# Performance work log

Measured on AMD Instinct MI355X. Metric: run time of the kernel, lower is better.

The kernel has to match this reference:

```python
import jax, jax.numpy as jnp
import numpy as np
import math

T = 4096        # block_size / sequence length
E = 2048        # embedding_dim
D = 256         # head_dim


def setup_inputs() -> dict:
    key = jax.random.key(0)
    k_x, k_q, k_k, k_v = jax.random.split(key, 4)
    x = jax.random.normal(k_x, (T, E), dtype=jnp.float32)
    # nn.Linear weights are [out_features, in_features]
    s = 1.0 / math.sqrt(E)
    Wq = jax.random.normal(k_q, (D, E), dtype=jnp.float32) * s
    Wk = jax.random.normal(k_k, (D, E), dtype=jnp.float32) * s
    Wv = jax.random.normal(k_v, (D, E), dtype=jnp.float32) * s
    return {"x": x, "Wq": Wq, "Wk": Wk, "Wv": Wv}


def reference(x, Wq, Wk, Wv):
    # Projections: x @ W.T  (torch Linear, no bias)
    Q = x @ Wq.T            # [T, D]
    K = x @ Wk.T            # [T, D]
    V = x @ Wv.T            # [T, D]
    scale = 1.0 / math.sqrt(Q.shape[-1])
    scores = (Q @ K.T) * scale                      # [T, T]
    causal = jnp.tril(jnp.ones((T, T), dtype=bool))
    scores = jnp.where(causal, scores, jnp.float32(-1e10))
    probs = jax.nn.softmax(scores, axis=-1)         # row softmax (torch legacy dim=1 for 2-D)
    return probs @ V                                # [T, D]
```

## Files before the change

kernel.cpp:

```cpp
#include <hip/hip_runtime.h>
#include <hip/hip_bf16.h>

#define T_DIM 4096
#define E_DIM 2048
#define D_DIM 256

typedef __attribute__((ext_vector_type(4))) float f32x4;
typedef __attribute__((ext_vector_type(8))) short s16x8;

__device__ __forceinline__ unsigned short f2bf(float f) {
  unsigned int u = __float_as_uint(f);
  unsigned int r = (u + 0x7FFFu + ((u >> 16) & 1u)) >> 16;
  return (unsigned short)r;
}
__device__ __forceinline__ float bf2f(unsigned short h) {
  return __uint_as_float(((unsigned int)h) << 16);
}

__device__ __forceinline__ f32x4 mfma16(s16x8 a, s16x8 b, f32x4 c) {
  return __builtin_amdgcn_mfma_f32_16x16x32_bf16(a, b, c, 0, 0, 0);
}

__device__ __forceinline__ void gload_lds16(const void* g, void* l) {
  __builtin_amdgcn_global_load_lds((const __attribute__((address_space(1))) void*)g,
                                   (__attribute__((address_space(3))) void*)l, 16, 0, 0);
}

__device__ __forceinline__ int fbase(int t) {
  int g = t / 3, r = t - 3 * g;
  return 3 * g * (g + 1) / 2 + r * (g + 1);
}

__global__ __launch_bounds__(256) void cvt_kernel(const float* __restrict__ src,
                                                  unsigned short* __restrict__ dst, int n) {
  int i = blockIdx.x * blockDim.x + threadIdx.x;
  if (i * 8 + 8 <= n) {
    float4 a = ((const float4*)src)[i * 2];
    float4 b = ((const float4*)src)[i * 2 + 1];
    uint4 o;
    o.x = (unsigned int)f2bf(a.x) | ((unsigned int)f2bf(a.y) << 16);
    o.y = (unsigned int)f2bf(a.z) | ((unsigned int)f2bf(a.w) << 16);
    o.z = (unsigned int)f2bf(b.x) | ((unsigned int)f2bf(b.y) << 16);
    o.w = (unsigned int)f2bf(b.z) | ((unsigned int)f2bf(b.w) << 16);
    ((uint4*)dst)[i] = o;
  }
}

__global__ __launch_bounds__(256, 3) void qkv_gemm(
    const unsigned short* __restrict__ xb, const unsigned short* __restrict__ wb,
    unsigned short* __restrict__ Qg, unsigned short* __restrict__ Kg,
    unsigned short* __restrict__ Vt) {
  __shared__ __align__(16) unsigned short Al[2][128 * 64];
  __shared__ __align__(16) unsigned short Bl[2][64 * 64];
  int tid = threadIdx.x, wid = tid >> 6, lane = tid & 63;
  int lr = lane & 15, lk = lane >> 4;
  int bi_ = (int)blockIdx.x;
  int xcd = bi_ & 7, kk = bi_ >> 3;
  int mb_ = (kk / 12) * 8 + xcd, nb_ = kk % 12;
  int bm0 = mb_ * 128, bn0 = nb_ * 64;
  int wm = (wid >> 1) * 64, wn = (wid & 1) * 32;

  f32x4 acc[4][2];
#pragma unroll
  for (int m = 0; m < 4; ++m)
#pragma unroll
    for (int n = 0; n < 2; ++n) acc[m][n] = (f32x4){0.f, 0.f, 0.f, 0.f};

#define STAGE_QKV(kt, buf)                                                              \
  {                                                                                     \
    int k0 = (kt)*64;                                                                   \
    _Pragma("unroll") for (int i2 = 0; i2 < 4; ++i2) {                                  \
      int ci = (wid * 4 + i2) * 64 + lane;                                              \
      int row = ci >> 3, cc = ci & 7;                                                   \
      gload_lds16(&xb[(size_t)(bm0 + row) * E_DIM + k0 + ((cc ^ (row & 7)) << 3)],      \
                  &Al[buf][(size_t)(wid * 4 + i2) * 512]);                              \
    }                                                                                   \
    _Pragma("unroll") for (int i2 = 0; i2 < 2; ++i2) {                                  \
      int ci = (wid * 2 + i2) * 64 + lane;                                              \
      int row = ci >> 3, cc = ci & 7;                                                   \
      gload_lds16(&wb[(size_t)(bn0 + row) * E_DIM + k0 + ((cc ^ (row & 7)) << 3)],      \
                  &Bl[buf][(size_t)(wid * 2 + i2) * 512]);                              \
    }                                                                                   \
  }

  STAGE_QKV(0, 0);
  for (int kt = 0; kt < 32; ++kt) {
    int cur = kt & 1;
    __syncthreads();
    if (kt + 1 < 32) STAGE_QKV(kt + 1, cur ^ 1);
    s16x8 af[2][4], bfr[2][2];
#pragma unroll
    for (int c = 0; c < 2; ++c) {
#pragma unroll
      for (int m = 0; m < 4; ++m)
        af[c][m] = *(const s16x8*)&Al[cur][(size_t)(wm + m * 16 + lr) * 64 +
                                           (((c * 4 + lk) ^ (lr & 7)) << 3)];
#pragma unroll
      for (int n = 0; n < 2; ++n)
        bfr[c][n] = *(const s16x8*)&Bl[cur][(size_t)(wn + n * 16 + lr) * 64 +
                                            (((c * 4 + lk) ^ (lr & 7)) << 3)];
    }
#pragma unroll
    for (int c = 0; c < 2; ++c)
#pragma unroll
      for (int m = 0; m < 4; ++m)
#pragma unroll
        for (int n = 0; n < 2; ++n) acc[m][n] = mfma16(af[c][m], bfr[c][n], acc[m][n]);
  }

#pragma unroll
  for (int m = 0; m < 4; ++m) {
    int grow = bm0 + wm + m * 16 + lk * 4;
#pragma unroll
    for (int n = 0; n < 2; ++n) {
      int gcol = bn0 + wn + n * 16 + lr;
      unsigned short h[4];
#pragma unroll
      for (int r = 0; r < 4; ++r) h[r] = f2bf(acc[m][n][r]);
      if (gcol < 256) {
#pragma unroll
        for (int r = 0; r < 4; ++r) Qg[(size_t)(grow + r) * D_DIM + gcol] = h[r];
      } else if (gcol < 512) {
#pragma unroll
        for (int r = 0; r < 4; ++r) Kg[(size_t)(grow + r) * D_DIM + gcol - 256] = h[r];
      } else {
        uint2 w;
        w.x = (unsigned int)h[0] | ((unsigned int)h[1] << 16);
        w.y = (unsigned int)h[2] | ((unsigned int)h[3] << 16);
        *(uint2*)&Vt[(size_t)(gcol - 512) * T_DIM + grow] = w;
      }
    }
  }
#undef STAGE_QKV
}

__global__ __launch_bounds__(256, 2) void attn_kernel(
    const unsigned short* __restrict__ Qg, const unsigned short* __restrict__ Kg,
    const unsigned short* __restrict__ Vt, unsigned short* __restrict__ Opart,
    float* __restrict__ mpart, float* __restrict__ lpart) {
  __shared__ __align__(16) unsigned short Kl[2][32 * 256];
  __shared__ __align__(16) unsigned short Vl[2][256 * 32];
  __shared__ __align__(16) unsigned short Pl[4][16 * 40];

  int b = blockIdx.x;
  int t = (int)sqrtf(6.0f * (float)b + 2.25f);
  if (t > 63) t = 63;
  while (t > 0 && fbase(t) > b) --t;
  while (t < 63 && fbase(t + 1) <= b) ++t;
  int s = b - fbase(t);
  int nt = 2 * t + 2 - 6 * s;
  if (nt > 6) nt = 6;

  int tid = threadIdx.x, wid = tid >> 6, lane = tid & 63;
  int lr = lane & 15, lk = lane >> 4;
  int q0 = t * 64 + wid * 16;
  unsigned short* pl = &Pl[wid][0];

  s16x8 qf[8];
#pragma unroll
  for (int c = 0; c < 8; ++c)
    qf[c] = *(const s16x8*)&Qg[(size_t)(q0 + lr) * D_DIM + c * 32 + lk * 8];

  float m_run = -1e30f, l_run = 0.0f;
  f32x4 Oa[16];
#pragma unroll
  for (int d = 0; d < 16; ++d) Oa[d] = (f32x4){0.f, 0.f, 0.f, 0.f};
  const float scale = 0.0625f;

#define STAGE_KV(j, buf)                                                             \
  {                                                                                  \
    int kv_ = (j)*32;                                                                \
    _Pragma("unroll") for (int i2 = 0; i2 < 4; ++i2) {                               \
      int ci = (wid * 4 + i2) * 64 + lane;                                           \
      int row = ci >> 5, cc = ci & 31;                                               \
      gload_lds16(&Kg[(size_t)(kv_ + row) * D_DIM + ((cc ^ (row & 7)) << 3)],        \
                  &Kl[buf][(size_t)(wid * 4 + i2) * 512]);                           \
    }                                                                                \
    _Pragma("unroll") for (int i2 = 0; i2 < 4; ++i2) {                               \
      int ci = (wid * 4 + i2) * 64 + lane;                                           \
      int rr = ci >> 2, cc = ci & 3;                                                 \
      gload_lds16(&Vt[(size_t)rr * T_DIM + kv_ + ((cc ^ ((rr >> 1) & 3)) << 3)],     \
                  &Vl[buf][(size_t)(wid * 4 + i2) * 512]);                           \
    }                                                                                \
  }

  STAGE_KV(6 * s, 0);
  for (int n = 0; n < nt; ++n) {
    int j = 6 * s + n;
    int kv = j * 32;
    int cur = n & 1;
    __syncthreads();
    if (n + 1 < nt) STAGE_KV(j + 1, cur ^ 1);
    const unsigned short* kl = &Kl[cur][0];
    const unsigned short* vl = &Vl[cur][0];

    f32x4 sa[2];
    sa[0] = (f32x4){0.f, 0.f, 0.f, 0.f};
    sa[1] = (f32x4){0.f, 0.f, 0.f, 0.f};
#pragma unroll
    for (int jb = 0; jb < 2; ++jb) {
      int row = jb * 16 + lr;
#pragma unroll
      for (int c = 0; c < 8; ++c) {
        s16x8 kf = *(const s16x8*)&kl[(size_t)row * 256 + (((c * 4 + lk) ^ (lr & 7)) << 3)];
        sa[jb] = mfma16(kf, qf[c], sa[jb]);
      }
    }

    float tmax = -1e30f;
#pragma unroll
    for (int jb = 0; jb < 2; ++jb) {
#pragma unroll
      for (int r = 0; r < 4; ++r) {
        float v = sa[jb][r] * scale;
        int keyg = kv + jb * 16 + lk * 4 + r;
        if (keyg > q0 + lr) v = -1e30f;
        sa[jb][r] = v;
        tmax = fmaxf(tmax, v);
      }
    }
    tmax = fmaxf(tmax, __shfl_xor(tmax, 16));
    tmax = fmaxf(tmax, __shfl_xor(tmax, 32));
    float m_new = fmaxf(fmaxf(m_run, tmax), -1e29f);
    float alpha = __expf(m_run - m_new);
    float psum = 0.f;
#pragma unroll
    for (int jb = 0; jb < 2; ++jb) {
      float p0 = __expf(sa[jb][0] - m_new);
      float p1 = __expf(sa[jb][1] - m_new);
      float p2 = __expf(sa[jb][2] - m_new);
      float p3 = __expf(sa[jb][3] - m_new);
      psum += (p0 + p1) + (p2 + p3);
      uint2 w;
      w.x = (unsigned int)f2bf(p0) | ((unsigned int)f2bf(p1) << 16);
      w.y = (unsigned int)f2bf(p2) | ((unsigned int)f2bf(p3) << 16);
      *(uint2*)&pl[lr * 40 + jb * 16 + lk * 4] = w;
    }
    psum += __shfl_xor(psum, 16);
    psum += __shfl_xor(psum, 32);
    l_run = l_run * alpha + psum;
    m_run = m_new;
    float al[4];
#pragma unroll
    for (int r = 0; r < 4; ++r) al[r] = __shfl(alpha, lk * 4 + r);
#pragma unroll
    for (int d = 0; d < 16; ++d) {
#pragma unroll
      for (int r = 0; r < 4; ++r) Oa[d][r] *= al[r];
    }

    s16x8 pf = *(const s16x8*)&pl[lr * 40 + lk * 8];
    int vsw = (lk ^ ((lr >> 1) & 3)) << 3;
#pragma unroll
    for (int d = 0; d < 16; ++d) {
      s16x8 vf = *(const s16x8*)&vl[(size_t)(d * 16 + lr) * 32 + vsw];
      Oa[d] = mfma16(pf, vf, Oa[d]);
    }
  }

#pragma unroll
  for (int d = 0; d < 16; ++d) {
    unsigned short h[4];
#pragma unroll
    for (int r = 0; r < 4; ++r) h[r] = f2bf(Oa[d][r]);
    uint2 w;
    w.x = (unsigned int)h[0] | ((unsigned int)h[1] << 16);
    w.y = (unsigned int)h[2] | ((unsigned int)h[3] << 16);
    *(uint2*)&Opart[((size_t)b * 256 + d * 16 + lr) * 64 + wid * 16 + lk * 4] = w;
  }
  if (lane < 16) {
    mpart[(size_t)b * 64 + wid * 16 + lr] = m_run;
    lpart[(size_t)b * 64 + wid * 16 + lr] = l_run;
  }
#undef STAGE_KV
}

__global__ __launch_bounds__(256) void merge_kernel(const unsigned short* __restrict__ Opart,
                                                    const float* __restrict__ mpart,
                                                    const float* __restrict__ lpart,
                                                    float* __restrict__ out) {
  __shared__ float trans[64 * 65];
  int blk = blockIdx.x;
  int t = blk >> 2;
  int d0 = (blk & 3) * 64;
  int q0 = t * 64;
  int ql = threadIdx.x & 63;
  int dg = threadIdx.x >> 6;
  int g = t / 3, r3 = t - 3 * g;
  int base = 3 * g * (g + 1) / 2 + r3 * (g + 1);
  int nb = (t + 3) / 3;

  float M = -1e30f, den = 0.f;
  for (int p = 0; p < nb; ++p) {
    float mp = mpart[(size_t)(base + p) * 64 + ql];
    float lp = lpart[(size_t)(base + p) * 64 + ql];
    float Mn = fmaxf(M, mp);
    float sc = __expf(M - Mn);
    den = den * sc + __expf(mp - Mn) * lp;
    M = Mn;
  }
  float inv = 1.0f / den;

  float acc[16];
#pragma unroll
  for (int k = 0; k < 16; ++k) acc[k] = 0.f;
  for (int p = 0; p < nb; ++p) {
    float w = __expf(mpart[(size_t)(base + p) * 64 + ql] - M);
    const unsigned short* oprow = &Opart[((size_t)(base + p) * 256 + d0 + dg) * 64 + ql];
#pragma unroll
    for (int k = 0; k < 16; ++k) acc[k] += w * bf2f(oprow[(size_t)(4 * k) * 64]);
  }
#pragma unroll
  for (int k = 0; k < 16; ++k) trans[(dg + 4 * k) * 65 + ql] = acc[k] * inv;
  __syncthreads();

#pragma unroll
  for (int k = 0; k < 16; ++k) {
    int qq = (threadIdx.x >> 6) + 4 * k;
    int dd = threadIdx.x & 63;
    out[(size_t)(q0 + qq) * 256 + d0 + dd] = trans[dd * 65 + qq];
  }
}

extern "C" void kernel_launch(void* const* d_in, const int* in_sizes, int n_in,
                              void* d_out, int out_size, void* d_ws, size_t ws_size,
                              hipStream_t stream) {
  const float* x  = (const float*)d_in[0];
  const float* Wq = (const float*)d_in[1];
  const float* Wk = (const float*)d_in[2];
  const float* Wv = (const float*)d_in[3];

  char* ws = (char*)d_ws;
  unsigned short* xb = (unsigned short*)(ws);
  unsigned short* wb = (unsigned short*)(ws + 16777216);
  unsigned short* Qg = (unsigned short*)(ws + 19922944);
  unsigned short* Kg = (unsigned short*)(ws + 22020096);
  unsigned short* Vt = (unsigned short*)(ws + 24117248);
  unsigned short* Opart = (unsigned short*)(ws + 26214400);
  float* mpart = (float*)(ws + 49643520);
  float* lpart = (float*)(ws + 49826560);

  cvt_kernel<<<4096, 256, 0, stream>>>(x, xb, T_DIM * E_DIM);
  cvt_kernel<<<256, 256, 0, stream>>>(Wq, wb, D_DIM * E_DIM);
  cvt_kernel<<<256, 256, 0, stream>>>(Wk, wb + (size_t)D_DIM * E_DIM, D_DIM * E_DIM);
  cvt_kernel<<<256, 256, 0, stream>>>(Wv, wb + (size_t)2 * D_DIM * E_DIM, D_DIM * E_DIM);

  qkv_gemm<<<384, 256, 0, stream>>>(xb, wb, Qg, Kg, Vt);

  attn_kernel<<<715, 256, 0, stream>>>(Qg, Kg, Vt, Opart, mpart, lpart);

  merge_kernel<<<256, 256, 0, stream>>>(Opart, mpart, lpart, (float*)d_out);
}
```

Before: 108.4 us.

## Double attention query tile per warp and fuse conversion kernels into one launch

Each attention wave now handles 32 query rows (two 16-row MFMA blocks) instead of 16, so each K/V fragment loaded from LDS feeds two MFMAs. The block tile grows to 128 queries, the split-KV partition changes to chunks of 5 key tiles (435 blocks), and the merge kernel is adapted to 128-row tiles. A mask-skip check avoids causal masking for tiles fully below the diagonal. The four fp32-to-bf16 conversion launches are merged into a single kernel. The trade-off is doubled accumulator registers and fewer blocks for load balancing.

```diff
diff --git a/kernel.cpp b/kernel.cpp
--- a/kernel.cpp
+++ b/kernel.cpp
@@ -4,6 +4,7 @@
 #define T_DIM 4096
 #define E_DIM 2048
 #define D_DIM 256
+#define NT_SPLIT 5
 
 typedef __attribute__((ext_vector_type(4))) float f32x4;
 typedef __attribute__((ext_vector_type(8))) short s16x8;
@@ -26,24 +27,29 @@
                                    (__attribute__((address_space(3))) void*)l, 16, 0, 0);
 }
 
-__device__ __forceinline__ int fbase(int t) {
-  int g = t / 3, r = t - 3 * g;
-  return 3 * g * (g + 1) / 2 + r * (g + 1);
-}
-
-__global__ __launch_bounds__(256) void cvt_kernel(const float* __restrict__ src,
-                                                  unsigned short* __restrict__ dst, int n) {
-  int i = blockIdx.x * blockDim.x + threadIdx.x;
-  if (i * 8 + 8 <= n) {
-    float4 a = ((const float4*)src)[i * 2];
-    float4 b = ((const float4*)src)[i * 2 + 1];
-    uint4 o;
-    o.x = (unsigned int)f2bf(a.x) | ((unsigned int)f2bf(a.y) << 16);
-    o.y = (unsigned int)f2bf(a.z) | ((unsigned int)f2bf(a.w) << 16);
-    o.z = (unsigned int)f2bf(b.x) | ((unsigned int)f2bf(b.y) << 16);
-    o.w = (unsigned int)f2bf(b.z) | ((unsigned int)f2bf(b.w) << 16);
-    ((uint4*)dst)[i] = o;
-  }
+__global__ __launch_bounds__(256) void cvt_all(const float* __restrict__ x,
+                                               const float* __restrict__ wq,
+                                               const float* __restrict__ wk,
+                                               const float* __restrict__ wv,
+                                               unsigned short* __restrict__ xb,
+                                               unsigned short* __restrict__ wb) {
+  int blk = blockIdx.x;
+  const float* src;
+  unsigned short* dst;
+  int rel;
+  if (blk < 4096)      { src = x;  dst = xb;           rel = blk; }
+  else if (blk < 4352) { src = wq; dst = wb;           rel = blk - 4096; }
+  else if (blk < 4608) { src = wk; dst = wb + 524288;  rel = blk - 4352; }
+  else                 { src = wv; dst = wb + 1048576; rel = blk - 4608; }
+  int i = rel * 256 + threadIdx.x;
+  float4 a = ((const float4*)src)[i * 2];
+  float4 b = ((const float4*)src)[i * 2 + 1];
+  uint4 o;
+  o.x = (unsigned int)f2bf(a.x) | ((unsigned int)f2bf(a.y) << 16);
+  o.y = (unsigned int)f2bf(a.z) | ((unsigned int)f2bf(a.w) << 16);
+  o.z = (unsigned int)f2bf(b.x) | ((unsigned int)f2bf(b.y) << 16);
+  o.w = (unsigned int)f2bf(b.z) | ((unsigned int)f2bf(b.w) << 16);
+  ((uint4*)dst)[i] = o;
 }
 
 __global__ __launch_bounds__(256, 3) void qkv_gemm(
@@ -140,137 +146,167 @@
     float* __restrict__ mpart, float* __restrict__ lpart) {
   __shared__ __align__(16) unsigned short Kl[2][32 * 256];
   __shared__ __align__(16) unsigned short Vl[2][256 * 32];
-  __shared__ __align__(16) unsigned short Pl[4][16 * 40];
+  __shared__ __align__(16) unsigned short Pl[4][32 * 40];
 
   int b = blockIdx.x;
-  int t = (int)sqrtf(6.0f * (float)b + 2.25f);
-  if (t > 63) t = 63;
-  while (t > 0 && fbase(t) > b) --t;
-  while (t < 63 && fbase(t + 1) <= b) ++t;
-  int s = b - fbase(t);
-  int nt = 2 * t + 2 - 6 * s;
-  if (nt > 6) nt = 6;
+  int t = 31, s = 0;
+  {
+    int acc = 0;
+#pragma unroll 1
+    for (int k = 1; k <= 32; ++k) {
+      int c = (4 * k + 4) / 5;
+      if (acc + c > b) { t = k - 1; s = b - acc; break; }
+      acc += c;
+    }
+  }
+  int nt = 4 * (t + 1) - NT_SPLIT * s;
+  if (nt > NT_SPLIT) nt = NT_SPLIT;
 
   int tid = threadIdx.x, wid = tid >> 6, lane = tid & 63;
   int lr = lane & 15, lk = lane >> 4;
-  int q0 = t * 64 + wid * 16;
+  int q0w = t * 128 + wid * 32;
   unsigned short* pl = &Pl[wid][0];
 
-  s16x8 qf[8];
-#pragma unroll
-  for (int c = 0; c < 8; ++c)
-    qf[c] = *(const s16x8*)&Qg[(size_t)(q0 + lr) * D_DIM + c * 32 + lk * 8];
-
-  float m_run = -1e30f, l_run = 0.0f;
-  f32x4 Oa[16];
-#pragma unroll
-  for (int d = 0; d < 16; ++d) Oa[d] = (f32x4){0.f, 0.f, 0.f, 0.f};
+  s16x8 qf[2][8];
+#pragma unroll
+  for (int qb = 0; qb < 2; ++qb)
+#pragma unroll
+    for (int c = 0; c < 8; ++c)
+      qf[qb][c] = *(const s16x8*)&Qg[(size_t)(q0w + qb * 16 + lr) * D_DIM + c * 32 + lk * 8];
+
+  float m_run[2] = {-1e30f, -1e30f}, l_run[2] = {0.f, 0.f};
+  f32x4 Oa[2][16];
+#pragma unroll
+  for (int qb = 0; qb < 2; ++qb)
+#pragma unroll
+    for (int d = 0; d < 16; ++d) Oa[qb][d] = (f32x4){0.f, 0.f, 0.f, 0.f};
   const float scale = 0.0625f;
+  int j0 = NT_SPLIT * s;
 
 #define STAGE_KV(j, buf)                                                             \
   {                                                                                  \
     int kv_ = (j)*32;                                                                \
     _Pragma("unroll") for (int i2 = 0; i2 < 4; ++i2) {                               \
-      int ci = (wid * 4 + i2) * 64 + lane;                                           \
-      int row = ci >> 5, cc = ci & 31;                                               \
-      gload_lds16(&Kg[(size_t)(kv_ + row) * D_DIM + ((cc ^ (row & 7)) << 3)],        \
+      int l = (wid * 4 + i2) * 64 + lane;                                            \
+      int row = l >> 5, gcs = l & 31;                                                \
+      gload_lds16(&Kg[(size_t)(kv_ + row) * D_DIM + ((gcs ^ (row & 7)) << 3)],       \
                   &Kl[buf][(size_t)(wid * 4 + i2) * 512]);                           \
     }                                                                                \
     _Pragma("unroll") for (int i2 = 0; i2 < 4; ++i2) {                               \
-      int ci = (wid * 4 + i2) * 64 + lane;                                           \
-      int rr = ci >> 2, cc = ci & 3;                                                 \
-      gload_lds16(&Vt[(size_t)rr * T_DIM + kv_ + ((cc ^ ((rr >> 1) & 3)) << 3)],     \
+      int l = (wid * 4 + i2) * 64 + lane;                                            \
+      int d_ = l >> 2, gs = l & 3;                                                   \
+      gload_lds16(&Vt[(size_t)d_ * T_DIM + kv_ + ((gs ^ ((d_ >> 1) & 3)) << 3)],     \
                   &Vl[buf][(size_t)(wid * 4 + i2) * 512]);                           \
     }                                                                                \
   }
 
-  STAGE_KV(6 * s, 0);
+  STAGE_KV(j0, 0);
   for (int n = 0; n < nt; ++n) {
-    int j = 6 * s + n;
-    int kv = j * 32;
-    int cur = n & 1;
+    int j = j0 + n, kv = j * 32, cur = n & 1;
     __syncthreads();
     if (n + 1 < nt) STAGE_KV(j + 1, cur ^ 1);
     const unsigned short* kl = &Kl[cur][0];
     const unsigned short* vl = &Vl[cur][0];
 
-    f32x4 sa[2];
-    sa[0] = (f32x4){0.f, 0.f, 0.f, 0.f};
-    sa[1] = (f32x4){0.f, 0.f, 0.f, 0.f};
+    f32x4 sa[2][2];
+#pragma unroll
+    for (int qb = 0; qb < 2; ++qb)
+#pragma unroll
+      for (int jb = 0; jb < 2; ++jb) sa[qb][jb] = (f32x4){0.f, 0.f, 0.f, 0.f};
+    int sw = lr & 7;
 #pragma unroll
     for (int jb = 0; jb < 2; ++jb) {
-      int row = jb * 16 + lr;
+      int rowbase = (jb * 16 + lr) * 32;
 #pragma unroll
       for (int c = 0; c < 8; ++c) {
-        s16x8 kf = *(const s16x8*)&kl[(size_t)row * 256 + (((c * 4 + lk) ^ (lr & 7)) << 3)];
-        sa[jb] = mfma16(kf, qf[c], sa[jb]);
-      }
-    }
-
-    float tmax = -1e30f;
-#pragma unroll
-    for (int jb = 0; jb < 2; ++jb) {
-#pragma unroll
-      for (int r = 0; r < 4; ++r) {
-        float v = sa[jb][r] * scale;
-        int keyg = kv + jb * 16 + lk * 4 + r;
-        if (keyg > q0 + lr) v = -1e30f;
-        sa[jb][r] = v;
-        tmax = fmaxf(tmax, v);
-      }
-    }
-    tmax = fmaxf(tmax, __shfl_xor(tmax, 16));
-    tmax = fmaxf(tmax, __shfl_xor(tmax, 32));
-    float m_new = fmaxf(fmaxf(m_run, tmax), -1e29f);
-    float alpha = __expf(m_run - m_new);
-    float psum = 0.f;
-#pragma unroll
-    for (int jb = 0; jb < 2; ++jb) {
-      float p0 = __expf(sa[jb][0] - m_new);
-      float p1 = __expf(sa[jb][1] - m_new);
-      float p2 = __expf(sa[jb][2] - m_new);
-      float p3 = __expf(sa[jb][3] - m_new);
-      psum += (p0 + p1) + (p2 + p3);
+        s16x8 kf = *(const s16x8*)&kl[(size_t)(rowbase + ((c * 4 + lk) ^ sw)) * 8];
+        sa[0][jb] = mfma16(kf, qf[0][c], sa[0][jb]);
+        sa[1][jb] = mfma16(kf, qf[1][c], sa[1][jb]);
+      }
+    }
+
+    bool needmask = (kv + 31 > q0w);
+    float alpha_s[2];
+#pragma unroll
+    for (int qb = 0; qb < 2; ++qb) {
+      int myq = q0w + qb * 16 + lr;
+      float tmax = -1e30f;
+#pragma unroll
+      for (int jb = 0; jb < 2; ++jb) {
+#pragma unroll
+        for (int r = 0; r < 4; ++r) {
+          float v = sa[qb][jb][r] * scale;
+          if (needmask && (kv + jb * 16 + lk * 4 + r) > myq) v = -1e30f;
+          sa[qb][jb][r] = v;
+          tmax = fmaxf(tmax, v);
+        }
+      }
+      tmax = fmaxf(tmax, __shfl_xor(tmax, 16));
+      tmax = fmaxf(tmax, __shfl_xor(tmax, 32));
+      float m_new = fmaxf(fmaxf(m_run[qb], tmax), -1e29f);
+      alpha_s[qb] = __expf(m_run[qb] - m_new);
+      float psum = 0.f;
+#pragma unroll
+      for (int jb = 0; jb < 2; ++jb) {
+        float p0 = __expf(sa[qb][jb][0] - m_new);
+        float p1 = __expf(sa[qb][jb][1] - m_new);
+        float p2 = __expf(sa[qb][jb][2] - m_new);
+        float p3 = __expf(sa[qb][jb][3] - m_new);
+        psum += (p0 + p1) + (p2 + p3);
+        uint2 w;
+        w.x = (unsigned int)f2bf(p0) | ((unsigned int)f2bf(p1) << 16);
+        w.y = (unsigned int)f2bf(p2) | ((unsigned int)f2bf(p3) << 16);
+        *(uint2*)&pl[(qb * 16 + lr) * 40 + jb * 16 + lk * 4] = w;
+      }
+      psum += __shfl_xor(psum, 16);
+      psum += __shfl_xor(psum, 32);
+      l_run[qb] = l_run[qb] * alpha_s[qb] + psum;
+      m_run[qb] = m_new;
+    }
+
+    float al[2][4];
+#pragma unroll
+    for (int qb = 0; qb < 2; ++qb)
+#pragma unroll
+      for (int r = 0; r < 4; ++r) al[qb][r] = __shfl(alpha_s[qb], lk * 4 + r);
+#pragma unroll
+    for (int qb = 0; qb < 2; ++qb)
+#pragma unroll
+      for (int d = 0; d < 16; ++d) {
+#pragma unroll
+        for (int r = 0; r < 4; ++r) Oa[qb][d][r] *= al[qb][r];
+      }
+
+    s16x8 pf0 = *(const s16x8*)&pl[lr * 40 + lk * 8];
+    s16x8 pf1 = *(const s16x8*)&pl[(16 + lr) * 40 + lk * 8];
+    int vsw = lk ^ ((lr >> 1) & 3);
+#pragma unroll
+    for (int d = 0; d < 16; ++d) {
+      s16x8 vf = *(const s16x8*)&vl[(size_t)((d * 16 + lr) * 4 + vsw) * 8];
+      Oa[0][d] = mfma16(pf0, vf, Oa[0][d]);
+      Oa[1][d] = mfma16(pf1, vf, Oa[1][d]);
+    }
+  }
+
+#pragma unroll
+  for (int d = 0; d < 16; ++d) {
+#pragma unroll
+    for (int qb = 0; qb < 2; ++qb) {
+      unsigned short h[4];
+#pragma unroll
+      for (int r = 0; r < 4; ++r) h[r] = f2bf(Oa[qb][d][r]);
       uint2 w;
-      w.x = (unsigned int)f2bf(p0) | ((unsigned int)f2bf(p1) << 16);
-      w.y = (unsigned int)f2bf(p2) | ((unsigned int)f2bf(p3) << 16);
-      *(uint2*)&pl[lr * 40 + jb * 16 + lk * 4] = w;
-    }
-    psum += __shfl_xor(psum, 16);
-    psum += __shfl_xor(psum, 32);
-    l_run = l_run * alpha + psum;
-    m_run = m_new;
-    float al[4];
-#pragma unroll
-    for (int r = 0; r < 4; ++r) al[r] = __shfl(alpha, lk * 4 + r);
-#pragma unroll
-    for (int d = 0; d < 16; ++d) {
-#pragma unroll
-      for (int r = 0; r < 4; ++r) Oa[d][r] *= al[r];
-    }
-
-    s16x8 pf = *(const s16x8*)&pl[lr * 40 + lk * 8];
-    int vsw = (lk ^ ((lr >> 1) & 3)) << 3;
-#pragma unroll
-    for (int d = 0; d < 16; ++d) {
-      s16x8 vf = *(const s16x8*)&vl[(size_t)(d * 16 + lr) * 32 + vsw];
-      Oa[d] = mfma16(pf, vf, Oa[d]);
-    }
-  }
-
-#pragma unroll
-  for (int d = 0; d < 16; ++d) {
-    unsigned short h[4];
-#pragma unroll
-    for (int r = 0; r < 4; ++r) h[r] = f2bf(Oa[d][r]);
-    uint2 w;
-    w.x = (unsigned int)h[0] | ((unsigned int)h[1] << 16);
-    w.y = (unsigned int)h[2] | ((unsigned int)h[3] << 16);
-    *(uint2*)&Opart[((size_t)b * 256 + d * 16 + lr) * 64 + wid * 16 + lk * 4] = w;
-  }
-  if (lane < 16) {
-    mpart[(size_t)b * 64 + wid * 16 + lr] = m_run;
-    lpart[(size_t)b * 64 + wid * 16 + lr] = l_run;
+      w.x = (unsigned int)h[0] | ((unsigned int)h[1] << 16);
+      w.y = (unsigned int)h[2] | ((unsigned int)h[3] << 16);
+      *(uint2*)&Opart[((size_t)b * 256 + d * 16 + lr) * 128 + wid * 32 + qb * 16 + lk * 4] = w;
+    }
+  }
+  if (lk == 0) {
+#pragma unroll
+    for (int qb = 0; qb < 2; ++qb) {
+      mpart[(size_t)b * 128 + wid * 32 + qb * 16 + lr] = m_run[qb];
+      lpart[(size_t)b * 128 + wid * 32 + qb * 16 + lr] = l_run[qb];
+    }
   }
 #undef STAGE_KV
 }
@@ -279,46 +315,43 @@
                                                     const float* __restrict__ mpart,
                                                     const float* __restrict__ lpart,
                                                     float* __restrict__ out) {
-  __shared__ float trans[64 * 65];
+  __shared__ float trans[128 * 65];
   int blk = blockIdx.x;
-  int t = blk >> 2;
-  int d0 = (blk & 3) * 64;
-  int q0 = t * 64;
-  int ql = threadIdx.x & 63;
-  int dg = threadIdx.x >> 6;
-  int g = t / 3, r3 = t - 3 * g;
-  int base = 3 * g * (g + 1) / 2 + r3 * (g + 1);
-  int nb = (t + 3) / 3;
+  int t = blk >> 2, d0 = (blk & 3) * 64, q0 = t * 128;
+  int ql = threadIdx.x & 127, dg = threadIdx.x >> 7;
+  int base = 0;
+#pragma unroll 1
+  for (int k = 1; k <= t; ++k) base += (4 * k + 4) / 5;
+  int nb = (4 * (t + 1) + 4) / 5;
 
   float M = -1e30f, den = 0.f;
   for (int p = 0; p < nb; ++p) {
-    float mp = mpart[(size_t)(base + p) * 64 + ql];
-    float lp = lpart[(size_t)(base + p) * 64 + ql];
+    float mp = mpart[(size_t)(base + p) * 128 + ql];
+    float lp = lpart[(size_t)(base + p) * 128 + ql];
     float Mn = fmaxf(M, mp);
-    float sc = __expf(M - Mn);
-    den = den * sc + __expf(mp - Mn) * lp;
+    den = den * __expf(M - Mn) + __expf(mp - Mn) * lp;
     M = Mn;
   }
   float inv = 1.0f / den;
 
-  float acc[16];
-#pragma unroll
-  for (int k = 0; k < 16; ++k) acc[k] = 0.f;
+  float acc[32];
+#pragma unroll
+  for (int k = 0; k < 32; ++k) acc[k] = 0.f;
   for (int p = 0; p < nb; ++p) {
-    float w = __expf(mpart[(size_t)(base + p) * 64 + ql] - M);
-    const unsigned short* oprow = &Opart[((size_t)(base + p) * 256 + d0 + dg) * 64 + ql];
-#pragma unroll
-    for (int k = 0; k < 16; ++k) acc[k] += w * bf2f(oprow[(size_t)(4 * k) * 64]);
-  }
-#pragma unroll
-  for (int k = 0; k < 16; ++k) trans[(dg + 4 * k) * 65 + ql] = acc[k] * inv;
+    float w = __expf(mpart[(size_t)(base + p) * 128 + ql] - M);
+    const unsigned short* op = &Opart[((size_t)(base + p) * 256 + d0 + dg) * 128 + ql];
+#pragma unroll
+    for (int k = 0; k < 32; ++k) acc[k] += w * bf2f(op[(size_t)(2 * k) * 128]);
+  }
+#pragma unroll
+  for (int k = 0; k < 32; ++k) trans[ql * 65 + dg + 2 * k] = acc[k] * inv;
   __syncthreads();
 
 #pragma unroll
-  for (int k = 0; k < 16; ++k) {
-    int qq = (threadIdx.x >> 6) + 4 * k;
+  for (int kk = 0; kk < 32; ++kk) {
+    int q = (threadIdx.x >> 6) + 4 * kk;
     int dd = threadIdx.x & 63;
-    out[(size_t)(q0 + qq) * 256 + d0 + dd] = trans[dd * 65 + qq];
+    out[(size_t)(q0 + q) * 256 + d0 + dd] = trans[q * 65 + dd];
   }
 }
 
@@ -337,17 +370,11 @@
   unsigned short* Kg = (unsigned short*)(ws + 22020096);
   unsigned short* Vt = (unsigned short*)(ws + 24117248);
   unsigned short* Opart = (unsigned short*)(ws + 26214400);
-  float* mpart = (float*)(ws + 49643520);
-  float* lpart = (float*)(ws + 49826560);
-
-  cvt_kernel<<<4096, 256, 0, stream>>>(x, xb, T_DIM * E_DIM);
-  cvt_kernel<<<256, 256, 0, stream>>>(Wq, wb, D_DIM * E_DIM);
-  cvt_kernel<<<256, 256, 0, stream>>>(Wk, wb + (size_t)D_DIM * E_DIM, D_DIM * E_DIM);
-  cvt_kernel<<<256, 256, 0, stream>>>(Wv, wb + (size_t)2 * D_DIM * E_DIM, D_DIM * E_DIM);
-
+  float* mpart = (float*)(ws + 54722560);
+  float* lpart = (float*)(ws + 54945280);
+
+  cvt_all<<<4864, 256, 0, stream>>>(x, Wq, Wk, Wv, xb, wb);
   qkv_gemm<<<384, 256, 0, stream>>>(xb, wb, Qg, Kg, Vt);
-
-  attn_kernel<<<715, 256, 0, stream>>>(Qg, Kg, Vt, Opart, mpart, lpart);
-
-  merge_kernel<<<256, 256, 0, stream>>>(Opart, mpart, lpart, (float*)d_out);
-}
+  attn_kernel<<<435, 256, 0, stream>>>(Qg, Kg, Vt, Opart, mpart, lpart);
+  merge_kernel<<<128, 256, 0, stream>>>(Opart, mpart, lpart, (float*)d_out);
+}
```

New measurement: 112.6 us. 1.04x slower.
